# Performance work log

Measured on AMD Instinct MI355X. Metric: run time of the kernel, lower is better.

The kernel has to match this reference:

```python
import jax, jax.numpy as jnp
import numpy as np

N = 50000   # nodes
E = 800000  # edges (before self-loops)
D = 96      # hidden_dim (= per-head out_channels, concat=False averages heads)
H = 4       # heads
L = 2       # num_layers
NEG_SLOPE = 0.2
EPS_BN = 1e-5


def setup_inputs() -> dict:
    key = jax.random.key(0)
    ks = jax.random.split(key, 8)
    x = jax.random.normal(ks[0], (N, D), dtype=jnp.float32)
    edge_index = jax.random.randint(ks[1], (2, E), 0, N, dtype=jnp.int64)
    # GATConv shared lin: in D -> H*D (per-head dim D), Glorot-ish scale
    W = jax.random.normal(ks[2], (L, D, H * D), dtype=jnp.float32) / np.sqrt(D).astype(np.float32)
    att_src = jax.random.normal(ks[3], (L, H, D), dtype=jnp.float32) * 0.1
    att_dst = jax.random.normal(ks[4], (L, H, D), dtype=jnp.float32) * 0.1
    bias = jnp.zeros((L, D), dtype=jnp.float32)
    gamma = jnp.ones((L, D), dtype=jnp.float32)
    beta = jnp.zeros((L, D), dtype=jnp.float32)
    return dict(x=x, edge_index=edge_index, W=W, att_src=att_src,
                att_dst=att_dst, bias=bias, gamma=gamma, beta=beta)


def _gat_layer(x, src, dst, W, a_src, a_dst, b):
    h = (x @ W).reshape(N, H, D)                      # [N,H,D]
    alpha_src = jnp.einsum('nhd,hd->nh', h, a_src)    # [N,H]
    alpha_dst = jnp.einsum('nhd,hd->nh', h, a_dst)    # [N,H]
    e = jax.nn.leaky_relu(alpha_src[src] + alpha_dst[dst], NEG_SLOPE)  # [Etot,H]
    # edge softmax grouped by destination node (numerically stable)
    m = jax.ops.segment_max(e, dst, num_segments=N)   # [N,H]
    p = jnp.exp(e - m[dst])
    denom = jax.ops.segment_sum(p, dst, num_segments=N)
    alpha = p / (denom[dst] + 1e-16)                  # [Etot,H]
    msg = h[src] * alpha[:, :, None]                  # [Etot,H,D]
    out = jax.ops.segment_sum(msg, dst, num_segments=N)  # [N,H,D]
    return out.mean(axis=1) + b                       # concat=False -> head mean


def reference(x, edge_index, W, att_src, att_dst, bias, gamma, beta):
    # PyG GATConv adds self-loops by default
    loops = jnp.arange(N, dtype=edge_index.dtype)
    ei = jnp.concatenate([edge_index, jnp.stack([loops, loops])], axis=1)
    src, dst = ei[0], ei[1]
    for l in range(L):
        x_res = x
        out = _gat_layer(x, src, dst, W[l], att_src[l], att_dst[l], bias[l])
        # BatchNorm over nodes (training-mode batch statistics, biased var)
        mu = out.mean(axis=0)
        var = out.var(axis=0)
        out = (out - mu) / jnp.sqrt(var + EPS_BN) * gamma[l] + beta[l]
        # dropout is identity at inference
        x = jax.nn.relu(out) + x_res
    return x
```

## Files before the change

### kernel.cpp

```cpp
#include <hip/hip_runtime.h>

#define DD 96
#define HH 4
#define HD 384
#define NEG_SLOPE 0.2f
#define NB_STATS 128
#define SCAN_BS 1024
#define WTC 400

typedef unsigned int uint;
typedef unsigned short ushort;
typedef __attribute__((ext_vector_type(8))) short bf16x8;
typedef __attribute__((ext_vector_type(4))) float f32x4;

__device__ inline uint pack2bf(float lo, float hi) {
    uint ulo = __float_as_uint(lo); ulo += 0x7fffu + ((ulo >> 16) & 1u);
    uint uhi = __float_as_uint(hi); uhi += 0x7fffu + ((uhi >> 16) & 1u);
    return (ulo >> 16) | (uhi & 0xffff0000u);
}
__device__ inline ushort f2bf(float f) {
    uint u = __float_as_uint(f);
    u += 0x7fffu + ((u >> 16) & 1u);
    return (ushort)(u >> 16);
}

__global__ void wa_kernel(const float* __restrict__ W, const float* __restrict__ att_src,
                          const float* __restrict__ att_dst, float* __restrict__ wa) {
    const int l = blockIdx.x / DD;
    const int k = blockIdx.x % DD;
    const int t = threadIdx.x;
    const float* Wr = W + ((size_t)l * DD + k) * HD;
    const float* as = att_src + (size_t)l * HD;
    const float* ad = att_dst + (size_t)l * HD;
    const bool hiHalf = t >= 32;
    float s0=0,s1=0,s2=0,s3=0,d0=0,d1=0,d2=0,d3=0;
    int c; float w, ps, pd;
    c = t;       w = Wr[c]; s0 = fmaf(w, as[c], s0); d0 = fmaf(w, ad[c], d0);
    c = t + 64;  w = Wr[c]; ps = w * as[c]; pd = w * ad[c];
    s0 += hiHalf ? 0.f : ps;  s1 += hiHalf ? ps : 0.f;
    d0 += hiHalf ? 0.f : pd;  d1 += hiHalf ? pd : 0.f;
    c = t + 128; w = Wr[c]; s1 = fmaf(w, as[c], s1); d1 = fmaf(w, ad[c], d1);
    c = t + 192; w = Wr[c]; s2 = fmaf(w, as[c], s2); d2 = fmaf(w, ad[c], d2);
    c = t + 256; w = Wr[c]; ps = w * as[c]; pd = w * ad[c];
    s2 += hiHalf ? 0.f : ps;  s3 += hiHalf ? ps : 0.f;
    d2 += hiHalf ? 0.f : pd;  d3 += hiHalf ? pd : 0.f;
    c = t + 320; w = Wr[c]; s3 = fmaf(w, as[c], s3); d3 = fmaf(w, ad[c], d3);
#pragma unroll
    for (int off = 32; off; off >>= 1) {
        s0 += __shfl_xor(s0, off); s1 += __shfl_xor(s1, off);
        s2 += __shfl_xor(s2, off); s3 += __shfl_xor(s3, off);
        d0 += __shfl_xor(d0, off); d1 += __shfl_xor(d1, off);
        d2 += __shfl_xor(d2, off); d3 += __shfl_xor(d3, off);
    }
    if (t == 0) {
        float* o = wa + ((size_t)l * DD + k) * 8;
        o[0]=s0; o[1]=d0; o[2]=s1; o[3]=d1; o[4]=s2; o[5]=d2; o[6]=s3; o[7]=d3;
    }
}

__global__ void wt_kernel(const float* __restrict__ W, const float* __restrict__ wa,
                          ushort* __restrict__ wt) {
    const int l = blockIdx.x / WTC;
    const int c = blockIdx.x % WTC;
    const int k = threadIdx.x;
    float v = 0.f;
    if (c < HD)        v = W[((size_t)l * DD + k) * HD + c];
    else if (c < HD+8) v = wa[((size_t)l * DD + k) * 8 + (c - HD)];
    wt[((size_t)l * WTC + c) * DD + k] = f2bf(v);
}

__global__ void __launch_bounds__(256) gemm_mfma_kernel(const float* __restrict__ x,
        const ushort* __restrict__ wt, uint* __restrict__ hp,
        float* __restrict__ asrc, float* __restrict__ adst, int N) {
    const int t = threadIdx.x;
    const int w = t >> 6;
    const int lane = t & 63;
    const int q = lane & 15, g = lane >> 4;
    const int base = blockIdx.x * 64 + w * 16;
    const int nA = min(base + q, N - 1);

    f32x4 acc[25];
#pragma unroll
    for (int i = 0; i < 25; i++) acc[i] = (f32x4){0.f, 0.f, 0.f, 0.f};

#pragma unroll
    for (int s = 0; s < 3; s++) {
        const float* xp = x + (size_t)nA * DD + s * 32 + g * 8;
        const float4 xa = *(const float4*)xp;
        const float4 xb = *(const float4*)(xp + 4);
        union { uint u[4]; bf16x8 v; } A;
        A.u[0] = pack2bf(xa.x, xa.y);
        A.u[1] = pack2bf(xa.z, xa.w);
        A.u[2] = pack2bf(xb.x, xb.y);
        A.u[3] = pack2bf(xb.z, xb.w);
#pragma unroll
        for (int tt = 0; tt < 25; tt++) {
            const ushort* wp = wt + (size_t)(tt * 16 + q) * DD + s * 32 + g * 8;
            union { uint4 u4; bf16x8 v; } B;
            B.u4 = *(const uint4*)wp;
            acc[tt] = __builtin_amdgcn_mfma_f32_16x16x32_bf16(A.v, B.v, acc[tt], 0, 0, 0);
        }
    }
#pragma unroll
    for (int r = 0; r < 4; r++) {
        const int node = base + g * 4 + r;
        if (node < N) {
            uint* hr = hp + (size_t)node * 192;
#pragma unroll
            for (int p = 0; p < 3; p++)
#pragma unroll
                for (int tt = 0; tt < 4; tt++)
                    hr[p * 64 + tt * 16 + q] = pack2bf(acc[p * 8 + tt][r], acc[p * 8 + tt + 4][r]);
            if (q < 8) {
                const float v = acc[24][r];
                if ((q & 1) == 0) asrc[node * 4 + (q >> 1)] = v;
                else              adst[node * 4 + (q >> 1)] = v;
            }
        }
    }
}

__global__ void count_kernel(const int* __restrict__ ei, int* __restrict__ deg, int E) {
    int i = blockIdx.x * blockDim.x + threadIdx.x;
    const int stride = gridDim.x * blockDim.x;
    for (; i < E; i += stride) atomicAdd(&deg[ei[E + i]], 1);
}

__global__ void scan1_kernel(const int* __restrict__ deg, int* __restrict__ locpre,
                             int* __restrict__ bsum, int N) {
    __shared__ int ts[256];
    const int t = threadIdx.x;
    const int base = blockIdx.x * SCAN_BS + t * 4;
    int e0 = 0, e1 = 0, e2 = 0, e3 = 0;
    if (base + 3 < N) {
        const int4 v = *(const int4*)(deg + base);
        e0 = v.x + 1; e1 = v.y + 1; e2 = v.z + 1; e3 = v.w + 1;
    } else {
        if (base     < N) e0 = deg[base]     + 1;
        if (base + 1 < N) e1 = deg[base + 1] + 1;
        if (base + 2 < N) e2 = deg[base + 2] + 1;
        if (base + 3 < N) e3 = deg[base + 3] + 1;
    }
    const int s = e0 + e1 + e2 + e3;
    ts[t] = s;
    __syncthreads();
    for (int off = 1; off < 256; off <<= 1) {
        const int u = (t >= off) ? ts[t - off] : 0;
        __syncthreads();
        ts[t] += u;
        __syncthreads();
    }
    const int ex = ts[t] - s;
    if (base + 3 < N) {
        *(int4*)(locpre + base) = make_int4(ex, ex + e0, ex + e0 + e1, ex + e0 + e1 + e2);
    } else if (base < N) {
        locpre[base] = ex;
        if (base + 1 < N) locpre[base + 1] = ex + e0;
        if (base + 2 < N) locpre[base + 2] = ex + e0 + e1;
    }
    if (t == 255) bsum[blockIdx.x] = ts[255];
}

__global__ void scan2_kernel(int* __restrict__ bsum, int* __restrict__ rowptr,
                             int NBLK, int N) {
    const int t = threadIdx.x;
    const int mine = (t < NBLK) ? bsum[t] : 0;
    int v = mine;
#pragma unroll
    for (int off = 1; off < 64; off <<= 1) {
        const int u = __shfl_up(v, off);
        if (t >= off) v += u;
    }
    if (t < NBLK) bsum[t] = v - mine;
    if (t == 63) rowptr[N] = v;
}

__global__ void scan3_kernel(const int* __restrict__ locpre, const int* __restrict__ bsum,
                             int* __restrict__ rowptr, int* __restrict__ cursor, int N) {
    const int base = blockIdx.x * SCAN_BS + threadIdx.x * 4;
    const int boff = bsum[blockIdx.x];
    if (base + 3 < N) {
        int4 v = *(const int4*)(locpre + base);
        v.x += boff; v.y += boff; v.z += boff; v.w += boff;
        *(int4*)(rowptr + base) = v;
        *(int4*)(cursor + base) = v;
    } else {
        for (int i = base; i < N; i++) {
            const int r = locpre[i] + boff;
            rowptr[i] = r; cursor[i] = r;
        }
    }
}

__global__ void scatter_kernel(const int* __restrict__ ei, int* __restrict__ cursor,
                               const int* __restrict__ rowptr, int* __restrict__ col,
                               int* __restrict__ dstarr, int E, int Etot) {
    int i = blockIdx.x * blockDim.x + threadIdx.x;
    const int stride = gridDim.x * blockDim.x;
    for (; i < Etot; i += stride) {
        if (i < E) {
            const int src = ei[i], dst = ei[E + i];
            const int pos = atomicAdd(&cursor[dst], 1);
            col[pos] = src;
            dstarr[pos] = dst;
        } else {
            const int n = i - E;
            const int pos = rowptr[n + 1] - 1;
            col[pos] = n;
            dstarr[pos] = n;
        }
    }
}

__global__ void ew_kernel(const int* __restrict__ col, const int* __restrict__ dstarr,
                          const float* __restrict__ asrc, const float* __restrict__ adst,
                          float4* __restrict__ ew4, int Etot) {
    int i = blockIdx.x * blockDim.x + threadIdx.x;
    const int stride = gridDim.x * blockDim.x;
    for (; i < Etot; i += stride) {
        const int s = col[i], d = dstarr[i];
        const float4 av = ((const float4*)asrc)[s];
        const float4 dv = ((const float4*)adst)[d];
        float e0 = av.x + dv.x, e1 = av.y + dv.y, e2 = av.z + dv.z, e3 = av.w + dv.w;
        e0 = e0 > 0.f ? e0 : NEG_SLOPE * e0;
        e1 = e1 > 0.f ? e1 : NEG_SLOPE * e1;
        e2 = e2 > 0.f ? e2 : NEG_SLOPE * e2;
        e3 = e3 > 0.f ? e3 : NEG_SLOPE * e3;
        ew4[i] = make_float4(__expf(e0), __expf(e1), __expf(e2), __expf(e3));
    }
}

#define EDGE_FMA(u0, u1, u2, w4)                                                      \
    { den0 += w4.x; den1 += w4.y; den2 += w4.z; den3 += w4.w;                         \
      const float cf1 = hi32 ? w4.y : w4.x;                                           \
      const float cf4 = hi32 ? w4.w : w4.z;                                           \
      acc0 = fmaf(__uint_as_float(u0 << 16), w4.x, acc0);                             \
      acc1 = fmaf(__uint_as_float(u0 & 0xffff0000u), cf1, acc1);                      \
      acc2 = fmaf(__uint_as_float(u1 << 16), w4.y, acc2);                             \
      acc3 = fmaf(__uint_as_float(u1 & 0xffff0000u), w4.z, acc3);                     \
      acc4 = fmaf(__uint_as_float(u2 << 16), cf4, acc4);                              \
      acc5 = fmaf(__uint_as_float(u2 & 0xffff0000u), w4.w, acc5); }

__global__ void agg_csr_kernel(const int* __restrict__ rowptr, const int* __restrict__ col,
                               const uint* __restrict__ hp, const float4* __restrict__ ew4,
                               const float* __restrict__ bias,
                               float* __restrict__ y, int N) {
    const int lane = threadIdx.x & 63;
    const bool hi32 = lane >= 32;
    const int n = (blockIdx.x * blockDim.x + threadIdx.x) >> 6;
    if (n >= N) return;
    const int beg = rowptr[n], endp = rowptr[n + 1];
    float acc0=0,acc1=0,acc2=0,acc3=0,acc4=0,acc5=0;
    float den0=0,den1=0,den2=0,den3=0;
    int e = beg;
    for (; e + 4 <= endp; e += 4) {
        const int s0 = col[e], s1 = col[e + 1], s2 = col[e + 2], s3 = col[e + 3];
        const float4 wA = ew4[e],     wB = ew4[e + 1];
        const float4 wC = ew4[e + 2], wD = ew4[e + 3];
        const uint* h0 = hp + (size_t)s0 * 192 + lane;
        const uint* h1 = hp + (size_t)s1 * 192 + lane;
        const uint* h2 = hp + (size_t)s2 * 192 + lane;
        const uint* h3 = hp + (size_t)s3 * 192 + lane;
        const uint u00 = h0[0], u01 = h0[64], u02 = h0[128];
        const uint u10 = h1[0], u11 = h1[64], u12 = h1[128];
        const uint u20 = h2[0], u21 = h2[64], u22 = h2[128];
        const uint u30 = h3[0], u31 = h3[64], u32 = h3[128];
        EDGE_FMA(u00, u01, u02, wA);
        EDGE_FMA(u10, u11, u12, wB);
        EDGE_FMA(u20, u21, u22, wC);
        EDGE_FMA(u30, u31, u32, wD);
    }
    for (; e < endp; e++) {
        const int s0 = col[e];
        const float4 wA = ew4[e];
        const uint* h0 = hp + (size_t)s0 * 192 + lane;
        const uint u00 = h0[0], u01 = h0[64], u02 = h0[128];
        EDGE_FMA(u00, u01, u02, wA);
    }
    const float r0 = 0.25f / (den0 + 1e-16f);
    const float r1 = 0.25f / (den1 + 1e-16f);
    const float r2 = 0.25f / (den2 + 1e-16f);
    const float r3 = 0.25f / (den3 + 1e-16f);
    const float rc1 = hi32 ? r1 : r0;
    const float rc4 = hi32 ? r3 : r2;
    const float A = acc0 * r0 + acc3 * r2;
    const float B = acc1 * rc1 + acc4 * rc4;
    const float C = acc2 * r1 + acc5 * r3;
    const float shB = __shfl_xor(B, 32);
    const float shC = __shfl_xor(C, 32);
    float* yr = y + (size_t)n * DD;
    yr[lane] = A + (hi32 ? shC : shB) + bias[lane];
    if (!hi32) yr[64 + lane] = B + shC + bias[64 + lane];
}

__global__ void bnstats_kernel(const float* __restrict__ y, float* __restrict__ pbuf,
                               int total4) {
    __shared__ float ps[384 * 4];
    __shared__ float qs[384 * 4];
    const int t = threadIdx.x;
    const int stride = gridDim.x * 384;
    float s0=0,s1=0,s2=0,s3=0,q0=0,q1=0,q2=0,q3=0;
    for (int i = blockIdx.x * 384 + t; i < total4; i += stride) {
        const float4 v = ((const float4*)y)[i];
        s0 += v.x; q0 = fmaf(v.x, v.x, q0);
        s1 += v.y; q1 = fmaf(v.y, v.y, q1);
        s2 += v.z; q2 = fmaf(v.z, v.z, q2);
        s3 += v.w; q3 = fmaf(v.w, v.w, q3);
    }
    ps[t*4+0]=s0; ps[t*4+1]=s1; ps[t*4+2]=s2; ps[t*4+3]=s3;
    qs[t*4+0]=q0; qs[t*4+1]=q1; qs[t*4+2]=q2; qs[t*4+3]=q3;
    __syncthreads();
    if (t < 192) {
        const int d = t % 96;
        const float* src = (t < 96) ? ps : qs;
        float r = 0.f;
#pragma unroll
        for (int m = 0; m < 16; m++) r += src[d + 96 * m];
        pbuf[blockIdx.x * 192 + t] = r;
    }
}

__global__ void bnfin_kernel(const float* __restrict__ pbuf, const float* __restrict__ gamma,
                             const float* __restrict__ beta, float* __restrict__ scsh, int N) {
    const int d = threadIdx.x;
    float s = 0.f, q = 0.f;
    for (int b = 0; b < NB_STATS; b++) {
        s += pbuf[b * 192 + d];
        q += pbuf[b * 192 + 96 + d];
    }
    const float invN = 1.f / (float)N;
    const float mu = s * invN;
    const float var = q * invN - mu * mu;
    const float sc = gamma[d] * rsqrtf(var + 1e-5f);
    scsh[d] = sc;
    scsh[d + DD] = beta[d] - mu * sc;
}

__global__ void bn_apply_kernel(const float* __restrict__ y, const float* __restrict__ scsh,
                                const float* __restrict__ xin, float* __restrict__ xout,
                                int total4) {
    int i = blockIdx.x * blockDim.x + threadIdx.x;
    const int stride = gridDim.x * blockDim.x;
    for (; i < total4; i += stride) {
        const int d4 = (i % 24) * 4;
        const float4 v = ((const float4*)y)[i];
        const float4 xi = ((const float4*)xin)[i];
        float4 o; float a;
        a = fmaf(v.x, scsh[d4],     scsh[d4 + DD]);     o.x = (a > 0.f ? a : 0.f) + xi.x;
        a = fmaf(v.y, scsh[d4 + 1], scsh[d4 + 1 + DD]); o.y = (a > 0.f ? a : 0.f) + xi.y;
        a = fmaf(v.z, scsh[d4 + 2], scsh[d4 + 2 + DD]); o.z = (a > 0.f ? a : 0.f) + xi.z;
        a = fmaf(v.w, scsh[d4 + 3], scsh[d4 + 3 + DD]); o.w = (a > 0.f ? a : 0.f) + xi.w;
        ((float4*)xout)[i] = o;
    }
}

extern "C" void kernel_launch(void* const* d_in, const int* in_sizes, int n_in,
                              void* d_out, int out_size, void* d_ws, size_t ws_size,
                              hipStream_t stream) {
    const float* x        = (const float*)d_in[0];
    const int*   ei       = (const int*)d_in[1];
    const float* W        = (const float*)d_in[2];
    const float* att_src  = (const float*)d_in[3];
    const float* att_dst  = (const float*)d_in[4];
    const float* bias     = (const float*)d_in[5];
    const float* gamma    = (const float*)d_in[6];
    const float* beta     = (const float*)d_in[7];
    float* out_final = (float*)d_out;

    const int N = in_sizes[0] / DD;
    const int E = in_sizes[1] / 2;
    const int Etot = E + N;
    const int NBLK = (N + SCAN_BS - 1) / SCAN_BS;

    char* ws = (char*)d_ws;
    size_t off = 0;
    auto alloc = [&](size_t bytes) -> void* {
        void* p = ws + off;
        off += (bytes + 255) & ~(size_t)255;
        return p;
    };
    uint*   hp     = (uint*)alloc((size_t)N * 192 * 4);
    float*  asrc   = (float*)alloc((size_t)N * HH * 4);
    float*  adst   = (float*)alloc((size_t)N * HH * 4);
    float*  y      = (float*)alloc((size_t)N * DD * 4);
    float*  xbuf   = (float*)alloc((size_t)N * DD * 4);
    float*  pbuf   = (float*)alloc((size_t)NB_STATS * 192 * 4);
    float*  scsh   = (float*)alloc(2 * DD * 4);
    float*  wa     = (float*)alloc(2 * DD * 8 * 4);
    ushort* wt     = (ushort*)alloc((size_t)2 * WTC * DD * 2);
    int*    deg    = (int*)alloc((size_t)N * 4);
    int*    locpre = (int*)alloc((size_t)N * 4);
    int*    bsum   = (int*)alloc(64 * 4);
    int*    rowptr = (int*)alloc((size_t)(N + 1) * 4);
    int*    cursor = (int*)alloc((size_t)N * 4);
    int*    colidx = (int*)alloc((size_t)Etot * 4);
    int*    dstarr = (int*)alloc((size_t)Etot * 4);
    float4* ew4    = (float4*)alloc((size_t)Etot * 16);

    hipMemsetAsync(deg, 0, (size_t)N * 4, stream);
    count_kernel<<<1024, 256, 0, stream>>>(ei, deg, E);
    scan1_kernel<<<NBLK, 256, 0, stream>>>(deg, locpre, bsum, N);
    scan2_kernel<<<1, 64, 0, stream>>>(bsum, rowptr, NBLK, N);
    scan3_kernel<<<NBLK, 256, 0, stream>>>(locpre, bsum, rowptr, cursor, N);
    scatter_kernel<<<1024, 256, 0, stream>>>(ei, cursor, rowptr, colidx, dstarr, E, Etot);
    wa_kernel<<<2 * DD, 64, 0, stream>>>(W, att_src, att_dst, wa);
    wt_kernel<<<2 * WTC, DD, 0, stream>>>(W, wa, wt);

    for (int l = 0; l < 2; l++) {
        const float* xin = (l == 0) ? x : xbuf;
        float* xout = (l == 1) ? out_final : xbuf;

        gemm_mfma_kernel<<<(N + 63) / 64, 256, 0, stream>>>(
            xin, wt + (size_t)l * WTC * DD, hp, asrc, adst, N);
        ew_kernel<<<2048, 256, 0, stream>>>(colidx, dstarr, asrc, adst, ew4, Etot);
        agg_csr_kernel<<<(N * 64 + 255) / 256, 256, 0, stream>>>(
            rowptr, colidx, hp, ew4, bias + (size_t)l * DD, y, N);
        bnstats_kernel<<<NB_STATS, 384, 0, stream>>>(y, pbuf, N * DD / 4);
        bnfin_kernel<<<1, DD, 0, stream>>>(pbuf, gamma + (size_t)l * DD,
                                           beta + (size_t)l * DD, scsh, N);
        bn_apply_kernel<<<2048, 256, 0, stream>>>(y, scsh, xin, xout, N * DD / 4);
    }
}
```

Before: 396.4 us.

## Fuse edge-weight compute into aggregation, BN-apply into next GEMM, merge scan kernels

Edge attention weights are now computed inside the aggregation kernel: each wave computes up to 64 exp-weights per chunk and stages them in LDS. This removes the separate ew kernel, the per-edge dstarr array and the 16-byte-per-edge weight buffer. Layer 1's BatchNorm apply, ReLU and residual are folded into the layer-2 GEMM's input load, which also writes the residual buffer. scan2 is merged into scan3 by having every block redo the small 64-entry prefix. The trade-off is extra launches and memory traffic removed in exchange for more work inside the aggregation loop, plus redundant scans.

```diff
diff --git a/kernel.cpp b/kernel.cpp
--- a/kernel.cpp
+++ b/kernel.cpp
@@ -69,7 +69,10 @@
     wt[((size_t)l * WTC + c) * DD + k] = f2bf(v);
 }
 
-__global__ void __launch_bounds__(256) gemm_mfma_kernel(const float* __restrict__ x,
+template<int FUSE>
+__global__ void __launch_bounds__(256) gemm_mfma_kernel(const float* __restrict__ xin,
+        const float* __restrict__ scsh, const float* __restrict__ xres,
+        float* __restrict__ xout,
         const ushort* __restrict__ wt, uint* __restrict__ hp,
         float* __restrict__ asrc, float* __restrict__ adst, int N) {
     const int t = threadIdx.x;
@@ -85,17 +88,41 @@
 
 #pragma unroll
     for (int s = 0; s < 3; s++) {
-        const float* xp = x + (size_t)nA * DD + s * 32 + g * 8;
-        const float4 xa = *(const float4*)xp;
-        const float4 xb = *(const float4*)(xp + 4);
+        const int kbase = s * 32 + g * 8;
+        float xv[8];
+        if (FUSE == 0) {
+            const float* xp = xin + (size_t)nA * DD + kbase;
+            const float4 xa = *(const float4*)xp;
+            const float4 xb = *(const float4*)(xp + 4);
+            xv[0]=xa.x; xv[1]=xa.y; xv[2]=xa.z; xv[3]=xa.w;
+            xv[4]=xb.x; xv[5]=xb.y; xv[6]=xb.z; xv[7]=xb.w;
+        } else {
+            const float* yp = xin + (size_t)nA * DD + kbase;
+            const float* rp = xres + (size_t)nA * DD + kbase;
+            const float4 ya = *(const float4*)yp;
+            const float4 yb = *(const float4*)(yp + 4);
+            const float4 ra = *(const float4*)rp;
+            const float4 rb = *(const float4*)(rp + 4);
+            const float yv[8] = {ya.x,ya.y,ya.z,ya.w,yb.x,yb.y,yb.z,yb.w};
+            const float rv[8] = {ra.x,ra.y,ra.z,ra.w,rb.x,rb.y,rb.z,rb.w};
+#pragma unroll
+            for (int j = 0; j < 8; j++) {
+                const int d = kbase + j;
+                float a = fmaf(yv[j], scsh[d], scsh[d + DD]);
+                xv[j] = (a > 0.f ? a : 0.f) + rv[j];
+            }
+            float* op = xout + (size_t)nA * DD + kbase;
+            *(float4*)op       = make_float4(xv[0], xv[1], xv[2], xv[3]);
+            *(float4*)(op + 4) = make_float4(xv[4], xv[5], xv[6], xv[7]);
+        }
         union { uint u[4]; bf16x8 v; } A;
-        A.u[0] = pack2bf(xa.x, xa.y);
-        A.u[1] = pack2bf(xa.z, xa.w);
-        A.u[2] = pack2bf(xb.x, xb.y);
-        A.u[3] = pack2bf(xb.z, xb.w);
+        A.u[0] = pack2bf(xv[0], xv[1]);
+        A.u[1] = pack2bf(xv[2], xv[3]);
+        A.u[2] = pack2bf(xv[4], xv[5]);
+        A.u[3] = pack2bf(xv[6], xv[7]);
 #pragma unroll
         for (int tt = 0; tt < 25; tt++) {
-            const ushort* wp = wt + (size_t)(tt * 16 + q) * DD + s * 32 + g * 8;
+            const ushort* wp = wt + (size_t)(tt * 16 + q) * DD + kbase;
             union { uint4 u4; bf16x8 v; } B;
             B.u4 = *(const uint4*)wp;
             acc[tt] = __builtin_amdgcn_mfma_f32_16x16x32_bf16(A.v, B.v, acc[tt], 0, 0, 0);
@@ -161,72 +188,52 @@
     if (t == 255) bsum[blockIdx.x] = ts[255];
 }
 
-__global__ void scan2_kernel(int* __restrict__ bsum, int* __restrict__ rowptr,
-                             int NBLK, int N) {
-    const int t = threadIdx.x;
-    const int mine = (t < NBLK) ? bsum[t] : 0;
-    int v = mine;
-#pragma unroll
-    for (int off = 1; off < 64; off <<= 1) {
-        const int u = __shfl_up(v, off);
-        if (t >= off) v += u;
-    }
-    if (t < NBLK) bsum[t] = v - mine;
-    if (t == 63) rowptr[N] = v;
-}
-
 __global__ void scan3_kernel(const int* __restrict__ locpre, const int* __restrict__ bsum,
-                             int* __restrict__ rowptr, int* __restrict__ cursor, int N) {
-    const int base = blockIdx.x * SCAN_BS + threadIdx.x * 4;
-    const int boff = bsum[blockIdx.x];
+                             int* __restrict__ rowptr, int* __restrict__ cursor,
+                             int N, int NBLK) {
+    __shared__ int s_boff, s_total;
+    const int t = threadIdx.x;
+    if (t < 64) {
+        const int mine = (t < NBLK) ? bsum[t] : 0;
+        int incl = mine;
+#pragma unroll
+        for (int off = 1; off < 64; off <<= 1) {
+            const int u = __shfl_up(incl, off);
+            if (t >= off) incl += u;
+        }
+        if (t == (int)blockIdx.x) s_boff = incl - mine;
+        if (t == NBLK - 1) s_total = incl;
+    }
+    __syncthreads();
+    const int boff = s_boff;
+    const int base = blockIdx.x * SCAN_BS + t * 4;
     if (base + 3 < N) {
         int4 v = *(const int4*)(locpre + base);
         v.x += boff; v.y += boff; v.z += boff; v.w += boff;
         *(int4*)(rowptr + base) = v;
         *(int4*)(cursor + base) = v;
     } else {
-        for (int i = base; i < N; i++) {
+        for (int i = base; i < N && i < base + 4; i++) {
             const int r = locpre[i] + boff;
             rowptr[i] = r; cursor[i] = r;
         }
     }
+    if (blockIdx.x == 0 && t == 0) rowptr[N] = s_total;
 }
 
 __global__ void scatter_kernel(const int* __restrict__ ei, int* __restrict__ cursor,
                                const int* __restrict__ rowptr, int* __restrict__ col,
-                               int* __restrict__ dstarr, int E, int Etot) {
+                               int E, int Etot) {
     int i = blockIdx.x * blockDim.x + threadIdx.x;
     const int stride = gridDim.x * blockDim.x;
     for (; i < Etot; i += stride) {
         if (i < E) {
             const int src = ei[i], dst = ei[E + i];
-            const int pos = atomicAdd(&cursor[dst], 1);
-            col[pos] = src;
-            dstarr[pos] = dst;
+            col[atomicAdd(&cursor[dst], 1)] = src;
         } else {
             const int n = i - E;
-            const int pos = rowptr[n + 1] - 1;
-            col[pos] = n;
-            dstarr[pos] = n;
-        }
-    }
-}
-
-__global__ void ew_kernel(const int* __restrict__ col, const int* __restrict__ dstarr,
-                          const float* __restrict__ asrc, const float* __restrict__ adst,
-                          float4* __restrict__ ew4, int Etot) {
-    int i = blockIdx.x * blockDim.x + threadIdx.x;
-    const int stride = gridDim.x * blockDim.x;
-    for (; i < Etot; i += stride) {
-        const int s = col[i], d = dstarr[i];
-        const float4 av = ((const float4*)asrc)[s];
-        const float4 dv = ((const float4*)adst)[d];
-        float e0 = av.x + dv.x, e1 = av.y + dv.y, e2 = av.z + dv.z, e3 = av.w + dv.w;
-        e0 = e0 > 0.f ? e0 : NEG_SLOPE * e0;
-        e1 = e1 > 0.f ? e1 : NEG_SLOPE * e1;
-        e2 = e2 > 0.f ? e2 : NEG_SLOPE * e2;
-        e3 = e3 > 0.f ? e3 : NEG_SLOPE * e3;
-        ew4[i] = make_float4(__expf(e0), __expf(e1), __expf(e2), __expf(e3));
+            col[rowptr[n + 1] - 1] = n;
+        }
     }
 }
 
@@ -241,41 +248,65 @@
       acc4 = fmaf(__uint_as_float(u2 << 16), cf4, acc4);                              \
       acc5 = fmaf(__uint_as_float(u2 & 0xffff0000u), w4.w, acc5); }
 
-__global__ void agg_csr_kernel(const int* __restrict__ rowptr, const int* __restrict__ col,
-                               const uint* __restrict__ hp, const float4* __restrict__ ew4,
-                               const float* __restrict__ bias,
-                               float* __restrict__ y, int N) {
-    const int lane = threadIdx.x & 63;
+__global__ void __launch_bounds__(256) agg_csr_kernel(
+        const int* __restrict__ rowptr, const int* __restrict__ col,
+        const uint* __restrict__ hp, const float* __restrict__ asrc,
+        const float* __restrict__ adst, const float* __restrict__ bias,
+        float* __restrict__ y, int N) {
+    __shared__ float4 wls[4][64];
+    __shared__ int    sls[4][64];
+    const int t = threadIdx.x;
+    const int lane = t & 63;
+    const int wv = t >> 6;
     const bool hi32 = lane >= 32;
-    const int n = (blockIdx.x * blockDim.x + threadIdx.x) >> 6;
+    const int n = (blockIdx.x * blockDim.x + t) >> 6;
     if (n >= N) return;
     const int beg = rowptr[n], endp = rowptr[n + 1];
+    const float4 adv = ((const float4*)adst)[n];
     float acc0=0,acc1=0,acc2=0,acc3=0,acc4=0,acc5=0;
     float den0=0,den1=0,den2=0,den3=0;
-    int e = beg;
-    for (; e + 4 <= endp; e += 4) {
-        const int s0 = col[e], s1 = col[e + 1], s2 = col[e + 2], s3 = col[e + 3];
-        const float4 wA = ew4[e],     wB = ew4[e + 1];
-        const float4 wC = ew4[e + 2], wD = ew4[e + 3];
-        const uint* h0 = hp + (size_t)s0 * 192 + lane;
-        const uint* h1 = hp + (size_t)s1 * 192 + lane;
-        const uint* h2 = hp + (size_t)s2 * 192 + lane;
-        const uint* h3 = hp + (size_t)s3 * 192 + lane;
-        const uint u00 = h0[0], u01 = h0[64], u02 = h0[128];
-        const uint u10 = h1[0], u11 = h1[64], u12 = h1[128];
-        const uint u20 = h2[0], u21 = h2[64], u22 = h2[128];
-        const uint u30 = h3[0], u31 = h3[64], u32 = h3[128];
-        EDGE_FMA(u00, u01, u02, wA);
-        EDGE_FMA(u10, u11, u12, wB);
-        EDGE_FMA(u20, u21, u22, wC);
-        EDGE_FMA(u30, u31, u32, wD);
-    }
-    for (; e < endp; e++) {
-        const int s0 = col[e];
-        const float4 wA = ew4[e];
-        const uint* h0 = hp + (size_t)s0 * 192 + lane;
-        const uint u00 = h0[0], u01 = h0[64], u02 = h0[128];
-        EDGE_FMA(u00, u01, u02, wA);
+
+    for (int cs = beg; cs < endp; cs += 64) {
+        const int cnt = min(64, endp - cs);
+        if (lane < cnt) {
+            const int s = col[cs + lane];
+            const float4 av = ((const float4*)asrc)[s];
+            float e0 = av.x + adv.x, e1 = av.y + adv.y;
+            float e2 = av.z + adv.z, e3 = av.w + adv.w;
+            e0 = e0 > 0.f ? e0 : NEG_SLOPE * e0;
+            e1 = e1 > 0.f ? e1 : NEG_SLOPE * e1;
+            e2 = e2 > 0.f ? e2 : NEG_SLOPE * e2;
+            e3 = e3 > 0.f ? e3 : NEG_SLOPE * e3;
+            sls[wv][lane] = s;
+            wls[wv][lane] = make_float4(__expf(e0), __expf(e1), __expf(e2), __expf(e3));
+        }
+        __builtin_amdgcn_wave_barrier();
+        int j = 0;
+        for (; j + 4 <= cnt; j += 4) {
+            const int4 sv = *(const int4*)&sls[wv][j];
+            const float4 wA = wls[wv][j],     wB = wls[wv][j + 1];
+            const float4 wC = wls[wv][j + 2], wD = wls[wv][j + 3];
+            const uint* h0 = hp + (size_t)sv.x * 192 + lane;
+            const uint* h1 = hp + (size_t)sv.y * 192 + lane;
+            const uint* h2 = hp + (size_t)sv.z * 192 + lane;
+            const uint* h3 = hp + (size_t)sv.w * 192 + lane;
+            const uint u00 = h0[0], u01 = h0[64], u02 = h0[128];
+            const uint u10 = h1[0], u11 = h1[64], u12 = h1[128];
+            const uint u20 = h2[0], u21 = h2[64], u22 = h2[128];
+            const uint u30 = h3[0], u31 = h3[64], u32 = h3[128];
+            EDGE_FMA(u00, u01, u02, wA);
+            EDGE_FMA(u10, u11, u12, wB);
+            EDGE_FMA(u20, u21, u22, wC);
+            EDGE_FMA(u30, u31, u32, wD);
+        }
+        for (; j < cnt; j++) {
+            const int s0 = sls[wv][j];
+            const float4 wA = wls[wv][j];
+            const uint* h0 = hp + (size_t)s0 * 192 + lane;
+            const uint u00 = h0[0], u01 = h0[64], u02 = h0[128];
+            EDGE_FMA(u00, u01, u02, wA);
+        }
+        __builtin_amdgcn_wave_barrier();
     }
     const float r0 = 0.25f / (den0 + 1e-16f);
     const float r1 = 0.25f / (den1 + 1e-16f);
@@ -394,30 +425,27 @@
     int*    rowptr = (int*)alloc((size_t)(N + 1) * 4);
     int*    cursor = (int*)alloc((size_t)N * 4);
     int*    colidx = (int*)alloc((size_t)Etot * 4);
-    int*    dstarr = (int*)alloc((size_t)Etot * 4);
-    float4* ew4    = (float4*)alloc((size_t)Etot * 16);
 
     hipMemsetAsync(deg, 0, (size_t)N * 4, stream);
     count_kernel<<<1024, 256, 0, stream>>>(ei, deg, E);
     scan1_kernel<<<NBLK, 256, 0, stream>>>(deg, locpre, bsum, N);
-    scan2_kernel<<<1, 64, 0, stream>>>(bsum, rowptr, NBLK, N);
-    scan3_kernel<<<NBLK, 256, 0, stream>>>(locpre, bsum, rowptr, cursor, N);
-    scatter_kernel<<<1024, 256, 0, stream>>>(ei, cursor, rowptr, colidx, dstarr, E, Etot);
+    scan3_kernel<<<NBLK, 256, 0, stream>>>(locpre, bsum, rowptr, cursor, N, NBLK);
+    scatter_kernel<<<1024, 256, 0, stream>>>(ei, cursor, rowptr, colidx, E, Etot);
     wa_kernel<<<2 * DD, 64, 0, stream>>>(W, att_src, att_dst, wa);
     wt_kernel<<<2 * WTC, DD, 0, stream>>>(W, wa, wt);
 
-    for (int l = 0; l < 2; l++) {
-        const float* xin = (l == 0) ? x : xbuf;
-        float* xout = (l == 1) ? out_final : xbuf;
-
-        gemm_mfma_kernel<<<(N + 63) / 64, 256, 0, stream>>>(
-            xin, wt + (size_t)l * WTC * DD, hp, asrc, adst, N);
-        ew_kernel<<<2048, 256, 0, stream>>>(colidx, dstarr, asrc, adst, ew4, Etot);
-        agg_csr_kernel<<<(N * 64 + 255) / 256, 256, 0, stream>>>(
-            rowptr, colidx, hp, ew4, bias + (size_t)l * DD, y, N);
-        bnstats_kernel<<<NB_STATS, 384, 0, stream>>>(y, pbuf, N * DD / 4);
-        bnfin_kernel<<<1, DD, 0, stream>>>(pbuf, gamma + (size_t)l * DD,
-                                           beta + (size_t)l * DD, scsh, N);
-        bn_apply_kernel<<<2048, 256, 0, stream>>>(y, scsh, xin, xout, N * DD / 4);
-    }
-}
+    gemm_mfma_kernel<0><<<(N + 63) / 64, 256, 0, stream>>>(
+        x, nullptr, nullptr, nullptr, wt, hp, asrc, adst, N);
+    agg_csr_kernel<<<(N * 64 + 255) / 256, 256, 0, stream>>>(
+        rowptr, colidx, hp, asrc, adst, bias, y, N);
+    bnstats_kernel<<<NB_STATS, 384, 0, stream>>>(y, pbuf, N * DD / 4);
+    bnfin_kernel<<<1, DD, 0, stream>>>(pbuf, gamma, beta, scsh, N);
+
+    gemm_mfma_kernel<1><<<(N + 63) / 64, 256, 0, stream>>>(
+        y, scsh, x, xbuf, wt + (size_t)WTC * DD, hp, asrc, adst, N);
+    agg_csr_kernel<<<(N * 64 + 255) / 256, 256, 0, stream>>>(
+        rowptr, colidx, hp, asrc, adst, bias + DD, y, N);
+    bnstats_kernel<<<NB_STATS, 384, 0, stream>>>(y, pbuf, N * DD / 4);
+    bnfin_kernel<<<1, DD, 0, stream>>>(pbuf, gamma + DD, beta + DD, scsh, N);
+    bn_apply_kernel<<<2048, 256, 0, stream>>>(y, scsh, xbuf, out_final, N * DD / 4);
+}
```

Result: no change. 396.3 us (-0.0%).
